# Optimization experiments

Hardware: AMD Instinct MI355X
Metric: run time of the kernel (lower is better)

## Reference

```python
import jax, jax.numpy as jnp
import numpy as np

B = 4
IN_DIM = 512
HID = 1024
MLP_LAYERS = 2
SEQ = 4096          # output_dim / sequence_length
RH = 64             # ripl_hidden_dim
RL = 2              # ripl_num_layers
MULT = 1            # ripl_coordinate_multipler

MID_DIM = 2 * RH * RH + (RH + 1) * RH      # per middle ripple layer param count
OUT_DIM = 2 * RH * 1 + (RH + 1) * 1        # output ripple layer param count
MLP_OUT = RL * MID_DIM + OUT_DIM


def gelu(x):
    return jax.nn.gelu(x, approximate=False)


def layer_norm(x, g, b, eps=1e-5):
    mu = jnp.mean(x, axis=-1, keepdims=True)
    var = jnp.var(x, axis=-1, keepdims=True)
    return (x - mu) * jax.lax.rsqrt(var + eps) * g + b


def batch_ripple(x, w, b):
    # x: (B,S,I), w: (B,O,I,2), b: (B,O,I+1)
    # out[b,s,o] = b[b,o,0] + sum_i b[b,o,i+1] * sin(w[b,o,i,0]*x[b,s,i] + w[b,o,i,1])
    arg = w[:, None, :, :, 0] * x[:, :, None, :] + w[:, None, :, :, 1]  # (B,S,O,I)
    return b[:, None, :, 0] + jnp.sum(jnp.sin(arg) * b[:, None, :, 1:], axis=-1)


def setup_inputs() -> dict:
    key = jax.random.key(0)
    ks = jax.random.split(key, 20)
    s = 0.02
    inp = {
        "x": jax.random.normal(ks[0], (B, IN_DIM), jnp.float32),
        "mlp_w0": jax.random.normal(ks[1], (IN_DIM, HID), jnp.float32) * s,
        "mlp_b0": jnp.zeros((HID,), jnp.float32),
        "mlp_w1": jax.random.normal(ks[2], (HID, HID), jnp.float32) * s,
        "mlp_b1": jnp.zeros((HID,), jnp.float32),
        "ln_g1": jnp.ones((HID,), jnp.float32),
        "ln_b1": jnp.zeros((HID,), jnp.float32),
        "mlp_w2": jax.random.normal(ks[3], (HID, HID), jnp.float32) * s,
        "mlp_b2": jnp.zeros((HID,), jnp.float32),
        "ln_g2": jnp.ones((HID,), jnp.float32),
        "ln_b2": jnp.zeros((HID,), jnp.float32),
        "mlp_w3": jax.random.normal(ks[4], (HID, MLP_OUT), jnp.float32) * s,
        "mlp_b3": jnp.zeros((MLP_OUT,), jnp.float32),
        "lc_w": jax.random.normal(ks[5], (1, RH), jnp.float32) * 0.1,
        "lc_b": jax.random.normal(ks[6], (RH,), jnp.float32) * 0.1,
        "byp_w": jax.random.normal(ks[7], (1, 1, 2), jnp.float32),
        "byp_b": jax.random.normal(ks[8], (1, 2), jnp.float32),
    }
    return inp


def reference(x, mlp_w0, mlp_b0, mlp_w1, mlp_b1, ln_g1, ln_b1,
              mlp_w2, mlp_b2, ln_g2, ln_b2, mlp_w3, mlp_b3,
              lc_w, lc_b, byp_w, byp_b):
    # hypernetwork MLP: Linear+GELU, [Linear+LN+GELU]*2, Linear
    h = gelu(x @ mlp_w0 + mlp_b0)
    h = gelu(layer_norm(h @ mlp_w1 + mlp_b1, ln_g1, ln_b1))
    h = gelu(layer_norm(h @ mlp_w2 + mlp_b2, ln_g2, ln_b2))
    mlp_out = h @ mlp_w3 + mlp_b3                      # (B, MLP_OUT)

    # split into RL middle ripple layers then the output layer
    middles = [mlp_out[:, i * MID_DIM:(i + 1) * MID_DIM] for i in range(RL)]
    out_w = mlp_out[:, RL * MID_DIM:RL * MID_DIM + OUT_DIM]

    # line coordinates -> fc layer
    lc = (jnp.arange(SEQ, dtype=jnp.float32) * MULT)[None, :, None]  # (1,S,1)
    lc = jnp.broadcast_to(lc, (x.shape[0], SEQ, 1))
    lc_x = lc @ lc_w + lc_b                                          # (B,S,RH)
    lc_bypass = lc_x

    for mw in middles:
        w = mw[:, :2 * RH * RH].reshape(-1, RH, RH, 2)
        b = mw[:, 2 * RH * RH:].reshape(-1, RH, RH + 1)
        lc_x = gelu(batch_ripple(lc_x, w, b))

    wo = out_w[:, :2 * RH].reshape(-1, 1, RH, 2)
    bo = out_w[:, 2 * RH:].reshape(-1, 1, RH + 1)
    lc_x = batch_ripple(lc_x, wo, bo)                                # (B,S,1)

    # learned RippleLinear(1,1) bypass, broadcast over features then reduced
    byp = byp_b[0, 0] + jnp.sum(
        jnp.sin(byp_w[0, 0, 0] * lc_bypass + byp_w[0, 0, 1]) * byp_b[0, 1],
        axis=-1, keepdims=True)
    lc_x = lc_x + byp
    return jnp.transpose(lc_x, (0, 2, 1))                            # (B,1,S)
```

## Files before the change

kernel.cpp:

```cpp
#include <hip/hip_runtime.h>
#include <math.h>

#define B_      4
#define IN_DIM  512
#define HID     1024
#define SEQ     4096
#define RH      64
#define RL      2
#define MID_DIM 12352
#define OUT_DIM 193
#define MLP_OUT 24897
#define INV2PI  0.15915494309189535f
#define MLPT_STRIDE 25088
#define KSPLIT3 16

#define OFF_P1    0
#define OFF_P2    65536
#define OFF_H2    131072
#define OFF_P3    135168
#define OFF_MLPT  1728576

__device__ __forceinline__ float gelu_exact(float v) {
    return 0.5f * v * (1.0f + erff(v * 0.70710678118654752f));
}

__device__ __forceinline__ float hw_sin_rev(float r) {
    r = r - __builtin_rintf(r);
    return __builtin_amdgcn_sinf(r);
}

__global__ void __launch_bounds__(256) k_A(
        const float* __restrict__ x,  const float* __restrict__ w0,
        const float* __restrict__ b0, const float* __restrict__ w1,
        float* __restrict__ p1) {
    const int cch = blockIdx.x, kc = blockIdx.y, tid = threadIdx.x;
    __shared__ __align__(16) float xs[B_ * IN_DIM];
    __shared__ float h0s[256];

    for (int e = tid; e < B_ * IN_DIM; e += 256) xs[e] = x[e];
    __syncthreads();

    {
        const int b = tid >> 6, kgl = tid & 63;
        const int kg = kc * 64 + kgl;
        const float* xp = xs + b * IN_DIM;
        const float* wp = w0 + kg;
        float acc = 0.f;
        #pragma unroll 8
        for (int k = 0; k < IN_DIM; ++k)
            acc = fmaf(xp[k], wp[(size_t)k * HID], acc);
        h0s[tid] = gelu_exact(acc + b0[kg]);
    }
    __syncthreads();

    {
        const int b = tid >> 6, cl = tid & 63;
        const int c = cch * 64 + cl;
        const float* wp = w1 + (size_t)(kc * 64) * HID + c;
        const float* hp = h0s + b * 64;
        float acc = 0.f;
        #pragma unroll 8
        for (int k = 0; k < 64; ++k)
            acc = fmaf(hp[k], wp[(size_t)k * HID], acc);
        p1[(kc * 4 + b) * HID + c] = acc;
    }
}

__global__ void __launch_bounds__(256) k_B(
        const float* __restrict__ p1, const float* __restrict__ b1,
        const float* __restrict__ g1, const float* __restrict__ bl1,
        const float* __restrict__ w2, float* __restrict__ p2) {
    const int cch = blockIdx.x, kc = blockIdx.y, tid = threadIdx.x;
    __shared__ float h1s[256];
    const int b = tid >> 6, lane = tid & 63;

    float s1 = 0.f, s2 = 0.f;
    #pragma unroll
    for (int q = 0; q < 16; ++q) {
        const int c = q * 64 + lane;
        float v = b1[c];
        #pragma unroll
        for (int j = 0; j < 16; ++j) v += p1[(j * 4 + b) * HID + c];
        s1 += v; s2 += v * v;
    }
    #pragma unroll
    for (int m = 1; m < 64; m <<= 1) {
        s1 += __shfl_xor(s1, m, 64);
        s2 += __shfl_xor(s2, m, 64);
    }
    const float mu = s1 * (1.0f / HID);
    const float rs = rsqrtf(s2 * (1.0f / HID) - mu * mu + 1e-5f);

    {
        const int k = kc * 64 + lane;
        float v = b1[k];
        #pragma unroll
        for (int j = 0; j < 16; ++j) v += p1[(j * 4 + b) * HID + k];
        h1s[tid] = gelu_exact((v - mu) * rs * g1[k] + bl1[k]);
    }
    __syncthreads();

    {
        const int c = cch * 64 + lane;
        const float* wp = w2 + (size_t)(kc * 64) * HID + c;
        const float* hp = h1s + b * 64;
        float acc = 0.f;
        #pragma unroll 8
        for (int k = 0; k < 64; ++k)
            acc = fmaf(hp[k], wp[(size_t)k * HID], acc);
        p2[(kc * 4 + b) * HID + c] = acc;
    }
}

__global__ void k_lng(const float* __restrict__ part, const float* __restrict__ bias,
                      const float* __restrict__ g, const float* __restrict__ bl,
                      float* __restrict__ h) {
    const int b = blockIdx.x, tid = threadIdx.x;
    float v = bias[tid];
    #pragma unroll
    for (int j = 0; j < 16; ++j) v += part[(j * 4 + b) * HID + tid];
    float s1 = v, s2 = v * v;
    #pragma unroll
    for (int m = 1; m < 64; m <<= 1) {
        s1 += __shfl_xor(s1, m, 64);
        s2 += __shfl_xor(s2, m, 64);
    }
    __shared__ float r1[16], r2[16], s_mu, s_rs;
    const int lane = tid & 63, wid = tid >> 6;
    if (lane == 0) { r1[wid] = s1; r2[wid] = s2; }
    __syncthreads();
    if (tid == 0) {
        float a = 0.f, c = 0.f;
        #pragma unroll
        for (int j = 0; j < 16; ++j) { a += r1[j]; c += r2[j]; }
        const float mu = a * (1.0f / HID);
        s_mu = mu;
        s_rs = rsqrtf(c * (1.0f / HID) - mu * mu + 1e-5f);
    }
    __syncthreads();
    h[b * HID + tid] = gelu_exact((v - s_mu) * s_rs * g[tid] + bl[tid]);
}

__global__ void __launch_bounds__(256) k_gemm3s(
        const float* __restrict__ h2, const float* __restrict__ w3,
        float* __restrict__ p3) {
    const int cch = blockIdx.x, kc = blockIdx.y, tid = threadIdx.x;
    __shared__ float hs[256];
    {
        const int b = tid >> 6, k = tid & 63;
        hs[tid] = h2[b * HID + kc * 64 + k];
    }
    __syncthreads();
    const int c = cch * 256 + tid;
    if (c >= MLP_OUT) return;
    const float* wp = w3 + (size_t)(kc * 64) * MLP_OUT + c;
    float a0 = 0.f, a1 = 0.f, a2 = 0.f, a3 = 0.f;
    #pragma unroll 16
    for (int k = 0; k < 64; ++k) {
        const float w = __builtin_nontemporal_load(&wp[(size_t)k * MLP_OUT]);
        a0 = fmaf(hs[k],       w, a0);
        a1 = fmaf(hs[64 + k],  w, a1);
        a2 = fmaf(hs[128 + k], w, a2);
        a3 = fmaf(hs[192 + k], w, a3);
    }
    p3[(size_t)(kc * 4 + 0) * MLP_OUT + c] = a0;
    p3[(size_t)(kc * 4 + 1) * MLP_OUT + c] = a1;
    p3[(size_t)(kc * 4 + 2) * MLP_OUT + c] = a2;
    p3[(size_t)(kc * 4 + 3) * MLP_OUT + c] = a3;
}

__global__ void k_comb3T(const float* __restrict__ p3, const float* __restrict__ b3,
                         float* __restrict__ mlpT) {
    const int d = blockIdx.x * 256 + threadIdx.x;
    const int b = blockIdx.y;
    int src = -1;
    float scale = 1.f;
    if (d < 24832) {
        const int l = d / 12416, r = d % 12416;
        const int base = l * MID_DIM;
        if (r < 8192) {
            const int half = r >> 12;
            const int rr = r & 4095;
            const int i = rr >> 6, o = rr & 63;
            src = base + o * 128 + i * 2 + half;
            scale = INV2PI;
        } else if (r < 12288) {
            const int rr = r - 8192;
            const int i = rr >> 6, o = rr & 63;
            src = base + 8192 + o * 65 + 1 + i;
        } else if (r < 12352) {
            const int o = r - 12288;
            src = base + 8192 + o * 65;
        }
    } else {
        const int rr = d - 24832;
        const int base = RL * MID_DIM;
        if (rr < 64)        { src = base + rr * 2;            scale = INV2PI; }
        else if (rr < 128)  { src = base + (rr - 64) * 2 + 1; scale = INV2PI; }
        else if (rr < 192)  { src = base + 128 + 1 + (rr - 128); }
        else if (rr == 192) { src = base + 128; }
    }
    float v = 0.f;
    if (src >= 0) {
        v = b3[src];
        #pragma unroll
        for (int j = 0; j < KSPLIT3; ++j)
            v += p3[(size_t)(j * 4 + b) * MLP_OUT + src];
        v *= scale;
    }
    mlpT[(size_t)b * MLPT_STRIDE + d] = v;
}

__global__ void __launch_bounds__(256, 2) k_ripple(
        const float* __restrict__ mlpT, const float* __restrict__ lcw,
        const float* __restrict__ lcb, const float* __restrict__ bypw,
        const float* __restrict__ bypb, float* __restrict__ out) {
    const int tid = threadIdx.x;
    const int b = blockIdx.y;
    const int t0 = blockIdx.x * 32;
    const int lane = tid & 63, wid = tid >> 6, tb = wid * 8;

    __shared__ __align__(16) float s_w[12416];
    __shared__ __align__(16) float s_x[64 * 36];
    __shared__ __align__(16) float s_wo[256];
    __shared__ float s_red[32];

    const float* mb = mlpT + (size_t)b * MLPT_STRIDE;

    {
        const float4* src = reinterpret_cast<const float4*>(mb);
        float4* dst = reinterpret_cast<float4*>(s_w);
        for (int e = tid; e < 3104; e += 256) dst[e] = src[e];
        if (tid < 64) {
            reinterpret_cast<float4*>(s_wo)[tid] =
                reinterpret_cast<const float4*>(mb + 24832)[tid];
        }
    }
    const float lw = lcw[lane], lb = lcb[lane];
    for (int e = tid; e < 2048; e += 256) {
        const int i = e >> 5, tt = e & 31;
        s_x[i * 36 + tt] = fmaf((float)(t0 + tt), lcw[i], lcb[i]);
    }
    __syncthreads();

    float acc[8];
    for (int layer = 0; layer < 2; ++layer) {
        const float bc = s_w[12288 + lane];
        #pragma unroll
        for (int j = 0; j < 8; ++j) acc[j] = bc;
        for (int i = 0; i < 64; ++i) {
            const float ws_ = s_w[i * 64 + lane];
            const float wo_ = s_w[4096 + i * 64 + lane];
            const float bs_ = s_w[8192 + i * 64 + lane];
            const float4 xa = *reinterpret_cast<const float4*>(&s_x[i * 36 + tb]);
            const float4 xb = *reinterpret_cast<const float4*>(&s_x[i * 36 + tb + 4]);
            const float xv[8] = {xa.x, xa.y, xa.z, xa.w, xb.x, xb.y, xb.z, xb.w};
            #pragma unroll
            for (int j = 0; j < 8; ++j) {
                const float r = fmaf(ws_, xv[j], wo_);
                acc[j] = fmaf(hw_sin_rev(r), bs_, acc[j]);
            }
        }
        __syncthreads();
        if (layer == 0) {
            #pragma unroll
            for (int j = 0; j < 8; ++j)
                s_x[lane * 36 + tb + j] = gelu_exact(acc[j]);
            const float4* src = reinterpret_cast<const float4*>(mb + 12416);
            float4* dst = reinterpret_cast<float4*>(s_w);
            for (int e = tid; e < 3104; e += 256) dst[e] = src[e];
            __syncthreads();
        }
    }

    {
        const float wsO = s_wo[lane], woO = s_wo[64 + lane], bsO = s_wo[128 + lane];
        const float bcO = s_wo[192];
        const float bw0 = bypw[0] * INV2PI, bw1 = bypw[1] * INV2PI;
        const float bb0 = bypb[0], bb1 = bypb[1];
        #pragma unroll
        for (int j = 0; j < 8; ++j) {
            const int t = t0 + tb + j;
            const float v = gelu_exact(acc[j]);
            float s = hw_sin_rev(fmaf(wsO, v, woO)) * bsO;
            const float xbv = fmaf((float)t, lw, lb);
            s = fmaf(hw_sin_rev(fmaf(bw0, xbv, bw1)), bb1, s);
            #pragma unroll
            for (int m = 1; m < 64; m <<= 1) s += __shfl_xor(s, m, 64);
            if (lane == 0) s_red[tb + j] = s + bcO + bb0;
        }
    }
    __syncthreads();
    if (tid < 32) out[(size_t)b * SEQ + t0 + tid] = s_red[tid];
}

extern "C" void kernel_launch(void* const* d_in, const int* in_sizes, int n_in,
                              void* d_out, int out_size, void* d_ws, size_t ws_size,
                              hipStream_t stream) {
    const float* x     = (const float*)d_in[0];
    const float* w0    = (const float*)d_in[1];
    const float* b0    = (const float*)d_in[2];
    const float* w1    = (const float*)d_in[3];
    const float* b1    = (const float*)d_in[4];
    const float* g1    = (const float*)d_in[5];
    const float* bln1  = (const float*)d_in[6];
    const float* w2    = (const float*)d_in[7];
    const float* b2    = (const float*)d_in[8];
    const float* g2    = (const float*)d_in[9];
    const float* bln2  = (const float*)d_in[10];
    const float* w3    = (const float*)d_in[11];
    const float* b3    = (const float*)d_in[12];
    const float* lcw   = (const float*)d_in[13];
    const float* lcb   = (const float*)d_in[14];
    const float* bypw  = (const float*)d_in[15];
    const float* bypb  = (const float*)d_in[16];
    float* out = (float*)d_out;
    float* ws  = (float*)d_ws;

    float* p1   = ws + OFF_P1;
    float* p2   = ws + OFF_P2;
    float* h2   = ws + OFF_H2;
    float* p3   = ws + OFF_P3;
    float* mlpT = ws + OFF_MLPT;

    k_A      <<<dim3(16, 16),       256, 0, stream>>>(x, w0, b0, w1, p1);
    k_B      <<<dim3(16, 16),       256, 0, stream>>>(p1, b1, g1, bln1, w2, p2);
    k_lng    <<<B_, 1024,           0, stream>>>(p2, b2, g2, bln2, h2);
    k_gemm3s <<<dim3(98, KSPLIT3),  256, 0, stream>>>(h2, w3, p3);
    k_comb3T <<<dim3(98, B_),       256, 0, stream>>>(p3, b3, mlpT);
    k_ripple <<<dim3(SEQ / 32, B_), 256, 0, stream>>>(mlpT, lcw, lcb, bypw, bypb, out);
}
```

Baseline: 282.8 us.

## Split first MLP layer and fuse final split-K reduce via atomics

The first MLP layer is split out of k_A into its own split-K GEMM kernel. Previously every k_A block recomputed the full x@w0 column slice over all 512 inputs, so w0 was read redundantly across blocks. The final GEMM now accumulates its split-K partials straight into the permuted, scaled mlpT buffer with float atomicAdd. That removes the p3 scratch buffer and the separate combine/transposition kernel, and the zeroing of mlpT is folded into the layernorm kernel. The cost is an extra kernel launch, atomic contention on mlpT, and a summation order that is no longer deterministic.

```diff
diff --git a/kernel.cpp b/kernel.cpp
--- a/kernel.cpp
+++ b/kernel.cpp
@@ -14,11 +14,11 @@
 #define MLPT_STRIDE 25088
 #define KSPLIT3 16
 
-#define OFF_P1    0
-#define OFF_P2    65536
-#define OFF_H2    131072
-#define OFF_P3    135168
-#define OFF_MLPT  1728576
+#define OFF_P0    0
+#define OFF_P1    32768
+#define OFF_P2    98304
+#define OFF_H2    163840
+#define OFF_MLPT  167936
 
 __device__ __forceinline__ float gelu_exact(float v) {
     return 0.5f * v * (1.0f + erff(v * 0.70710678118654752f));
@@ -29,41 +29,50 @@
     return __builtin_amdgcn_sinf(r);
 }
 
-__global__ void __launch_bounds__(256) k_A(
-        const float* __restrict__ x,  const float* __restrict__ w0,
-        const float* __restrict__ b0, const float* __restrict__ w1,
-        float* __restrict__ p1) {
+__global__ void __launch_bounds__(256) k_gemm0(
+        const float* __restrict__ x, const float* __restrict__ w0,
+        float* __restrict__ p0) {
     const int cch = blockIdx.x, kc = blockIdx.y, tid = threadIdx.x;
-    __shared__ __align__(16) float xs[B_ * IN_DIM];
-    __shared__ float h0s[256];
-
-    for (int e = tid; e < B_ * IN_DIM; e += 256) xs[e] = x[e];
-    __syncthreads();
-
-    {
-        const int b = tid >> 6, kgl = tid & 63;
-        const int kg = kc * 64 + kgl;
-        const float* xp = xs + b * IN_DIM;
-        const float* wp = w0 + kg;
-        float acc = 0.f;
-        #pragma unroll 8
-        for (int k = 0; k < IN_DIM; ++k)
-            acc = fmaf(xp[k], wp[(size_t)k * HID], acc);
-        h0s[tid] = gelu_exact(acc + b0[kg]);
-    }
-    __syncthreads();
-
-    {
-        const int b = tid >> 6, cl = tid & 63;
-        const int c = cch * 64 + cl;
-        const float* wp = w1 + (size_t)(kc * 64) * HID + c;
-        const float* hp = h0s + b * 64;
-        float acc = 0.f;
-        #pragma unroll 8
-        for (int k = 0; k < 64; ++k)
-            acc = fmaf(hp[k], wp[(size_t)k * HID], acc);
-        p1[(kc * 4 + b) * HID + c] = acc;
-    }
+    __shared__ float xs[256];
+    {
+        const int b = tid >> 6, k = tid & 63;
+        xs[tid] = x[b * IN_DIM + kc * 64 + k];
+    }
+    __syncthreads();
+    const int b = tid >> 6, cl = tid & 63;
+    const int c = cch * 64 + cl;
+    const float* wp = w0 + (size_t)(kc * 64) * HID + c;
+    const float* xp = xs + b * 64;
+    float acc = 0.f;
+    #pragma unroll 8
+    for (int k = 0; k < 64; ++k)
+        acc = fmaf(xp[k], wp[(size_t)k * HID], acc);
+    p0[(kc * 4 + b) * HID + c] = acc;
+}
+
+__global__ void __launch_bounds__(256) k_gemm1(
+        const float* __restrict__ p0, const float* __restrict__ b0,
+        const float* __restrict__ w1, float* __restrict__ p1) {
+    const int cch = blockIdx.x, kc = blockIdx.y, tid = threadIdx.x;
+    __shared__ float hs[256];
+    {
+        const int b = tid >> 6, k = tid & 63;
+        const int kg = kc * 64 + k;
+        float v = b0[kg];
+        #pragma unroll
+        for (int j = 0; j < 8; ++j) v += p0[(j * 4 + b) * HID + kg];
+        hs[tid] = gelu_exact(v);
+    }
+    __syncthreads();
+    const int b = tid >> 6, cl = tid & 63;
+    const int c = cch * 64 + cl;
+    const float* wp = w1 + (size_t)(kc * 64) * HID + c;
+    const float* hp = hs + b * 64;
+    float acc = 0.f;
+    #pragma unroll 8
+    for (int k = 0; k < 64; ++k)
+        acc = fmaf(hp[k], wp[(size_t)k * HID], acc);
+    p1[(kc * 4 + b) * HID + c] = acc;
 }
 
 __global__ void __launch_bounds__(256) k_B(
@@ -112,10 +121,14 @@
     }
 }
 
-__global__ void k_lng(const float* __restrict__ part, const float* __restrict__ bias,
-                      const float* __restrict__ g, const float* __restrict__ bl,
-                      float* __restrict__ h) {
+__global__ void k_lngz(const float* __restrict__ part, const float* __restrict__ bias,
+                       const float* __restrict__ g, const float* __restrict__ bl,
+                       float* __restrict__ h, float* __restrict__ mlpT) {
     const int b = blockIdx.x, tid = threadIdx.x;
+    {
+        float* mz = mlpT + (size_t)b * MLPT_STRIDE;
+        for (int e = tid; e < MLPT_STRIDE; e += 1024) mz[e] = 0.f;
+    }
     float v = bias[tid];
     #pragma unroll
     for (int j = 0; j < 16; ++j) v += part[(j * 4 + b) * HID + tid];
@@ -141,9 +154,9 @@
     h[b * HID + tid] = gelu_exact((v - s_mu) * s_rs * g[tid] + bl[tid]);
 }
 
-__global__ void __launch_bounds__(256) k_gemm3s(
+__global__ void __launch_bounds__(256) k_gemm3a(
         const float* __restrict__ h2, const float* __restrict__ w3,
-        float* __restrict__ p3) {
+        const float* __restrict__ b3, float* __restrict__ mlpT) {
     const int cch = blockIdx.x, kc = blockIdx.y, tid = threadIdx.x;
     __shared__ float hs[256];
     {
@@ -157,58 +170,38 @@
     float a0 = 0.f, a1 = 0.f, a2 = 0.f, a3 = 0.f;
     #pragma unroll 16
     for (int k = 0; k < 64; ++k) {
-        const float w = __builtin_nontemporal_load(&wp[(size_t)k * MLP_OUT]);
+        const float w = wp[(size_t)k * MLP_OUT];
         a0 = fmaf(hs[k],       w, a0);
         a1 = fmaf(hs[64 + k],  w, a1);
         a2 = fmaf(hs[128 + k], w, a2);
         a3 = fmaf(hs[192 + k], w, a3);
     }
-    p3[(size_t)(kc * 4 + 0) * MLP_OUT + c] = a0;
-    p3[(size_t)(kc * 4 + 1) * MLP_OUT + c] = a1;
-    p3[(size_t)(kc * 4 + 2) * MLP_OUT + c] = a2;
-    p3[(size_t)(kc * 4 + 3) * MLP_OUT + c] = a3;
-}
-
-__global__ void k_comb3T(const float* __restrict__ p3, const float* __restrict__ b3,
-                         float* __restrict__ mlpT) {
-    const int d = blockIdx.x * 256 + threadIdx.x;
-    const int b = blockIdx.y;
-    int src = -1;
-    float scale = 1.f;
-    if (d < 24832) {
-        const int l = d / 12416, r = d % 12416;
-        const int base = l * MID_DIM;
+    if (kc == 0) {
+        const float bb = b3[c];
+        a0 += bb; a1 += bb; a2 += bb; a3 += bb;
+    }
+    int d; float scale = 1.f;
+    if (c < RL * MID_DIM) {
+        const int l = c / MID_DIM, r = c % MID_DIM;
         if (r < 8192) {
-            const int half = r >> 12;
-            const int rr = r & 4095;
-            const int i = rr >> 6, o = rr & 63;
-            src = base + o * 128 + i * 2 + half;
+            const int o = r >> 7, rem = r & 127;
+            d = l * 12416 + (rem & 1) * 4096 + (rem >> 1) * 64 + o;
             scale = INV2PI;
-        } else if (r < 12288) {
-            const int rr = r - 8192;
-            const int i = rr >> 6, o = rr & 63;
-            src = base + 8192 + o * 65 + 1 + i;
-        } else if (r < 12352) {
-            const int o = r - 12288;
-            src = base + 8192 + o * 65;
+        } else {
+            const int u = r - 8192;
+            const int o = u / 65, idx = u % 65;
+            d = l * 12416 + (idx == 0 ? 12288 + o : 8192 + (idx - 1) * 64 + o);
         }
     } else {
-        const int rr = d - 24832;
-        const int base = RL * MID_DIM;
-        if (rr < 64)        { src = base + rr * 2;            scale = INV2PI; }
-        else if (rr < 128)  { src = base + (rr - 64) * 2 + 1; scale = INV2PI; }
-        else if (rr < 192)  { src = base + 128 + 1 + (rr - 128); }
-        else if (rr == 192) { src = base + 128; }
-    }
-    float v = 0.f;
-    if (src >= 0) {
-        v = b3[src];
-        #pragma unroll
-        for (int j = 0; j < KSPLIT3; ++j)
-            v += p3[(size_t)(j * 4 + b) * MLP_OUT + src];
-        v *= scale;
-    }
-    mlpT[(size_t)b * MLPT_STRIDE + d] = v;
+        const int u = c - RL * MID_DIM;
+        if (u < 128)      { d = 24832 + (u & 1) * 64 + (u >> 1); scale = INV2PI; }
+        else if (u == 128){ d = 24832 + 192; }
+        else              { d = 24832 + 128 + (u - 129); }
+    }
+    atomicAdd(&mlpT[(size_t)0 * MLPT_STRIDE + d], a0 * scale);
+    atomicAdd(&mlpT[(size_t)1 * MLPT_STRIDE + d], a1 * scale);
+    atomicAdd(&mlpT[(size_t)2 * MLPT_STRIDE + d], a2 * scale);
+    atomicAdd(&mlpT[(size_t)3 * MLPT_STRIDE + d], a3 * scale);
 }
 
 __global__ void __launch_bounds__(256, 2) k_ripple(
@@ -317,16 +310,16 @@
     float* out = (float*)d_out;
     float* ws  = (float*)d_ws;
 
+    float* p0   = ws + OFF_P0;
     float* p1   = ws + OFF_P1;
     float* p2   = ws + OFF_P2;
     float* h2   = ws + OFF_H2;
-    float* p3   = ws + OFF_P3;
     float* mlpT = ws + OFF_MLPT;
 
-    k_A      <<<dim3(16, 16),       256, 0, stream>>>(x, w0, b0, w1, p1);
+    k_gemm0  <<<dim3(16, 8),        256, 0, stream>>>(x, w0, p0);
+    k_gemm1  <<<dim3(16, 16),       256, 0, stream>>>(p0, b0, w1, p1);
     k_B      <<<dim3(16, 16),       256, 0, stream>>>(p1, b1, g1, bln1, w2, p2);
-    k_lng    <<<B_, 1024,           0, stream>>>(p2, b2, g2, bln2, h2);
-    k_gemm3s <<<dim3(98, KSPLIT3),  256, 0, stream>>>(h2, w3, p3);
-    k_comb3T <<<dim3(98, B_),       256, 0, stream>>>(p3, b3, mlpT);
+    k_lngz   <<<B_, 1024,           0, stream>>>(p2, b2, g2, bln2, h2, mlpT);
+    k_gemm3a <<<dim3(98, KSPLIT3),  256, 0, stream>>>(h2, w3, b3, mlpT);
     k_ripple <<<dim3(SEQ / 32, B_), 256, 0, stream>>>(mlpT, lcw, lcb, bypw, bypb, out);
 }
```

After: 313.0 us. +10.7%, slower.

## Split first MLP layer into separate split-K GEMM kernel, drop nontemporal loads

Applied to the files above, without the earlier changes.

The fused first kernel made every one of its 256 blocks recompute a 64-column slice of the first layer over the full input dimension, so each w0 slice was read 16 times. The first layer now runs as its own split-K GEMM writing partial sums. The second GEMM sums those partials, adds the bias and applies GELU before its own product. This adds one kernel launch and an intermediate buffer round trip, and shifts the workspace offsets. The w3 loads also change from nontemporal to ordinary loads.

```diff
diff --git a/kernel.cpp b/kernel.cpp
--- a/kernel.cpp
+++ b/kernel.cpp
@@ -14,11 +14,12 @@
 #define MLPT_STRIDE 25088
 #define KSPLIT3 16
 
-#define OFF_P1    0
-#define OFF_P2    65536
-#define OFF_H2    131072
-#define OFF_P3    135168
-#define OFF_MLPT  1728576
+#define OFF_P0    0
+#define OFF_P1    32768
+#define OFF_P2    98304
+#define OFF_H2    163840
+#define OFF_P3    167936
+#define OFF_MLPT  1761344
 
 __device__ __forceinline__ float gelu_exact(float v) {
     return 0.5f * v * (1.0f + erff(v * 0.70710678118654752f));
@@ -29,41 +30,50 @@
     return __builtin_amdgcn_sinf(r);
 }
 
-__global__ void __launch_bounds__(256) k_A(
-        const float* __restrict__ x,  const float* __restrict__ w0,
-        const float* __restrict__ b0, const float* __restrict__ w1,
-        float* __restrict__ p1) {
+__global__ void __launch_bounds__(256) k_gemm0(
+        const float* __restrict__ x, const float* __restrict__ w0,
+        float* __restrict__ p0) {
     const int cch = blockIdx.x, kc = blockIdx.y, tid = threadIdx.x;
-    __shared__ __align__(16) float xs[B_ * IN_DIM];
-    __shared__ float h0s[256];
-
-    for (int e = tid; e < B_ * IN_DIM; e += 256) xs[e] = x[e];
-    __syncthreads();
-
-    {
-        const int b = tid >> 6, kgl = tid & 63;
-        const int kg = kc * 64 + kgl;
-        const float* xp = xs + b * IN_DIM;
-        const float* wp = w0 + kg;
-        float acc = 0.f;
-        #pragma unroll 8
-        for (int k = 0; k < IN_DIM; ++k)
-            acc = fmaf(xp[k], wp[(size_t)k * HID], acc);
-        h0s[tid] = gelu_exact(acc + b0[kg]);
-    }
-    __syncthreads();
-
-    {
-        const int b = tid >> 6, cl = tid & 63;
-        const int c = cch * 64 + cl;
-        const float* wp = w1 + (size_t)(kc * 64) * HID + c;
-        const float* hp = h0s + b * 64;
-        float acc = 0.f;
-        #pragma unroll 8
-        for (int k = 0; k < 64; ++k)
-            acc = fmaf(hp[k], wp[(size_t)k * HID], acc);
-        p1[(kc * 4 + b) * HID + c] = acc;
-    }
+    __shared__ float xs[256];
+    {
+        const int b = tid >> 6, k = tid & 63;
+        xs[tid] = x[b * IN_DIM + kc * 64 + k];
+    }
+    __syncthreads();
+    const int b = tid >> 6, cl = tid & 63;
+    const int c = cch * 64 + cl;
+    const float* wp = w0 + (size_t)(kc * 64) * HID + c;
+    const float* xp = xs + b * 64;
+    float acc = 0.f;
+    #pragma unroll 8
+    for (int k = 0; k < 64; ++k)
+        acc = fmaf(xp[k], wp[(size_t)k * HID], acc);
+    p0[(kc * 4 + b) * HID + c] = acc;
+}
+
+__global__ void __launch_bounds__(256) k_gemm1(
+        const float* __restrict__ p0, const float* __restrict__ b0,
+        const float* __restrict__ w1, float* __restrict__ p1) {
+    const int cch = blockIdx.x, kc = blockIdx.y, tid = threadIdx.x;
+    __shared__ float hs[256];
+    {
+        const int b = tid >> 6, k = tid & 63;
+        const int kg = kc * 64 + k;
+        float v = b0[kg];
+        #pragma unroll
+        for (int j = 0; j < 8; ++j) v += p0[(j * 4 + b) * HID + kg];
+        hs[tid] = gelu_exact(v);
+    }
+    __syncthreads();
+    const int b = tid >> 6, cl = tid & 63;
+    const int c = cch * 64 + cl;
+    const float* wp = w1 + (size_t)(kc * 64) * HID + c;
+    const float* hp = hs + b * 64;
+    float acc = 0.f;
+    #pragma unroll 8
+    for (int k = 0; k < 64; ++k)
+        acc = fmaf(hp[k], wp[(size_t)k * HID], acc);
+    p1[(kc * 4 + b) * HID + c] = acc;
 }
 
 __global__ void __launch_bounds__(256) k_B(
@@ -157,7 +167,7 @@
     float a0 = 0.f, a1 = 0.f, a2 = 0.f, a3 = 0.f;
     #pragma unroll 16
     for (int k = 0; k < 64; ++k) {
-        const float w = __builtin_nontemporal_load(&wp[(size_t)k * MLP_OUT]);
+        const float w = wp[(size_t)k * MLP_OUT];
         a0 = fmaf(hs[k],       w, a0);
         a1 = fmaf(hs[64 + k],  w, a1);
         a2 = fmaf(hs[128 + k], w, a2);
@@ -317,13 +327,15 @@
     float* out = (float*)d_out;
     float* ws  = (float*)d_ws;
 
+    float* p0   = ws + OFF_P0;
     float* p1   = ws + OFF_P1;
     float* p2   = ws + OFF_P2;
     float* h2   = ws + OFF_H2;
     float* p3   = ws + OFF_P3;
     float* mlpT = ws + OFF_MLPT;
 
-    k_A      <<<dim3(16, 16),       256, 0, stream>>>(x, w0, b0, w1, p1);
+    k_gemm0  <<<dim3(16, 8),        256, 0, stream>>>(x, w0, p0);
+    k_gemm1  <<<dim3(16, 16),       256, 0, stream>>>(p0, b0, w1, p1);
     k_B      <<<dim3(16, 16),       256, 0, stream>>>(p1, b1, g1, bln1, w2, p2);
     k_lng    <<<B_, 1024,           0, stream>>>(p2, b2, g2, bln2, h2);
     k_gemm3s <<<dim3(98, KSPLIT3),  256, 0, stream>>>(h2, w3, p3);
```

Measured after the change: 259.9 us, median of 2. -8.1%, faster.
